# Kernel optimization log

Measured on AMD Instinct MI355X. Metric: run time of the kernel, lower is better.

Reference implementation:

```python
import jax, jax.numpy as jnp
import numpy as np

B, IN_DIM, MEM = 8192, 4096, 256
MIN_TS, MAX_TS, EPS = 0.1, 10.0, 1e-6
LN_EPS = 1e-5


def setup_inputs() -> dict:
    key = jax.random.key(0)
    ks = jax.random.split(key, 10)
    std = 0.02
    d_in = MEM + IN_DIM  # 4352
    return {
        "x": jax.random.normal(ks[0], (B, IN_DIM), jnp.float32),
        "h": jax.random.normal(ks[1], (B, MEM), jnp.float32),
        # memory_target: Linear(d_in, 2*MEM) -> LN -> GELU -> Linear(2*MEM, MEM)
        "W1": std * jax.random.normal(ks[2], (d_in, 2 * MEM), jnp.float32),
        "b1": jnp.zeros((2 * MEM,), jnp.float32),
        "g1": jnp.ones((2 * MEM,), jnp.float32),
        "be1": jnp.zeros((2 * MEM,), jnp.float32),
        "W2": std * jax.random.normal(ks[3], (2 * MEM, MEM), jnp.float32),
        "b2": jnp.zeros((MEM,), jnp.float32),
        # decay_gate: Linear(d_in, MEM) -> sigmoid
        "Wd": std * jax.random.normal(ks[4], (d_in, MEM), jnp.float32),
        "bd": jnp.zeros((MEM,), jnp.float32),
        # input_gate: Linear(d_in, MEM) -> sigmoid
        "Wu": std * jax.random.normal(ks[5], (d_in, MEM), jnp.float32),
        "bu": jnp.zeros((MEM,), jnp.float32),
    }


def _layernorm(t, g, b):
    mu = jnp.mean(t, axis=-1, keepdims=True)
    var = jnp.mean(jnp.square(t - mu), axis=-1, keepdims=True)
    return (t - mu) * jax.lax.rsqrt(var + LN_EPS) * g + b


def reference(x, h, W1, b1, g1, be1, W2, b2, Wd, bd, Wu, bu):
    combined = jnp.concatenate([h, x], axis=-1)  # [B, MEM+IN_DIM]
    # memory_target branch: Linear -> LayerNorm -> GELU (exact) -> Linear -> tanh
    t = _layernorm(combined @ W1 + b1, g1, be1)
    t = jax.nn.gelu(t, approximate=False)
    h_candidate = jnp.tanh(t @ W2 + b2)  # [B, MEM]
    # gates
    decay = jax.nn.sigmoid(combined @ Wd + bd)
    update = jax.nn.sigmoid(combined @ Wu + bu)
    decay = MIN_TS + (MAX_TS - MIN_TS) * decay + EPS
    new_h = (1.0 - update) * (h / decay) + update * h_candidate
    # normalize_memory: rescale new_h to old h's L2 norm
    h_norm = jnp.maximum(jnp.linalg.norm(h, axis=-1, keepdims=True), EPS)
    nh_norm = jnp.maximum(jnp.linalg.norm(new_h, axis=-1, keepdims=True), 1e-12)
    new_h = new_h / nh_norm * h_norm
    return new_h
```

## Files before the change

### kernel.cpp

```cpp
#include <hip/hip_runtime.h>
#include <stdint.h>

typedef unsigned short u16;

#define B_ROWS 8192
#define IN_DIM 4096
#define MEM 256
#define D_IN 4352
#define N1 1024
#define K2 512
#define LN_EPS 1e-5f

typedef __attribute__((ext_vector_type(4))) float f32x4;
typedef __attribute__((ext_vector_type(4))) uint32_t u32x4;
typedef __attribute__((ext_vector_type(4))) unsigned short u16x4;
typedef __attribute__((ext_vector_type(8))) short bf16x8;

#define AS1(p) ((__attribute__((address_space(1))) void*)(p))
#define AS3(p) ((__attribute__((address_space(3))) void*)(p))

__device__ __forceinline__ float bf2f(u16 u) {
  union { uint32_t u; float f; } c; c.u = ((uint32_t)u) << 16; return c.f;
}
__device__ __forceinline__ u16 f2bf(float f) {
  union { float f; uint32_t u; } c; c.f = f;
  uint32_t r = (c.u + 0x7fffu + ((c.u >> 16) & 1u)) >> 16;
  return (u16)r;
}
__device__ __forceinline__ uint32_t fbits(float f) {
  union { float f; uint32_t u; } c; c.f = f; return c.u;
}
__device__ __forceinline__ uint32_t pack_rne(float a, float b) {
  return ((uint32_t)f2bf(b) << 16) | f2bf(a);
}
__device__ __forceinline__ uint32_t pack_trunc(float a, float b) {
  return (fbits(b) & 0xFFFF0000u) | (fbits(a) >> 16);
}

__global__ __launch_bounds__(256)
void prep_kernel(const float* __restrict__ W1, const float* __restrict__ Wd,
                 const float* __restrict__ Wu, const float* __restrict__ W2,
                 const float* __restrict__ h, const float* __restrict__ x,
                 u16* __restrict__ WT, u16* __restrict__ W2F, u16* __restrict__ Abf) {
  __shared__ u16 tile[64][68];
  const int blk = blockIdx.x, t = threadIdx.x;
  if (blk < 1088) {
    int n0 = (blk & 15) * 64, k0 = (blk >> 4) * 64;
    const float* src; int srcN, ns0;
    if (n0 < 512)      { src = W1; srcN = 512; ns0 = n0; }
    else if (n0 < 768) { src = Wd; srcN = 256; ns0 = n0 - 512; }
    else               { src = Wu; srcN = 256; ns0 = n0 - 768; }
    int rr = t >> 4;
    int c4 = (t & 15) * 4;
#pragma unroll
    for (int i = 0; i < 4; i++) {
      int k = i * 16 + rr;
      f32x4 v = *(const f32x4*)&src[(size_t)(k0 + k) * srcN + ns0 + c4];
      tile[c4 + 0][k] = f2bf(v[0]);
      tile[c4 + 1][k] = f2bf(v[1]);
      tile[c4 + 2][k] = f2bf(v[2]);
      tile[c4 + 3][k] = f2bf(v[3]);
    }
    __syncthreads();
#pragma unroll
    for (int i = 0; i < 4; i++) {
      int n = i * 16 + rr;
      u16x4 w;
      w.x = tile[n][c4 + 0];
      w.y = tile[n][c4 + 1];
      w.z = tile[n][c4 + 2];
      w.w = tile[n][c4 + 3];
      *(u16x4*)&WT[(size_t)(n0 + n) * D_IN + k0 + c4] = w;
    }
  } else if (blk < 1104) {
    int kw = blk - 1088;
#pragma unroll
    for (int q = 0; q < 4; q++) {
      float v[8];
#pragma unroll
      for (int j = 0; j < 8; j++)
        v[j] = W2[(size_t)(kw * 32 + q * 8 + j) * 256 + t];
      u32x4 w;
      w.x = pack_rne(v[0], v[1]);
      w.y = pack_rne(v[2], v[3]);
      w.z = pack_rne(v[4], v[5]);
      w.w = pack_rne(v[6], v[7]);
      *(u32x4*)&W2F[(size_t)((kw * 4 + q) * 256 + t) * 8] = w;
    }
  } else {
    int b = blk - 1104;
    const float* src; int r, dcol;
    if (b < 1024) {
      int g = (b * 256 + t) * 8;
      src = h + g; r = g >> 8; dcol = g & 255;
    } else {
      int g = ((b - 1024) * 256 + t) * 8;
      src = x + g; r = g >> 12; dcol = MEM + (g & 4095);
    }
    f32x4 v0 = *(const f32x4*)src;
    f32x4 v1 = *(const f32x4*)(src + 4);
    u32x4 w;
    w.x = pack_rne(v0[0], v0[1]);
    w.y = pack_rne(v0[2], v0[3]);
    w.z = pack_rne(v1[0], v1[1]);
    w.w = pack_rne(v1[2], v1[3]);
    *(u32x4*)&Abf[(size_t)r * D_IN + dcol] = w;
  }
}

#define BAR() { asm volatile("" ::: "memory"); __builtin_amdgcn_s_barrier(); asm volatile("" ::: "memory"); }
#define VMW4() asm volatile("s_waitcnt vmcnt(4)" ::: "memory");
#define VMW0() asm volatile("s_waitcnt vmcnt(0)" ::: "memory");

__global__ __launch_bounds__(512, 2)
void gemm1_pre256_kernel(const u16* __restrict__ Abf, const u16* __restrict__ WT,
                         u16* __restrict__ G0, u16* __restrict__ G1, int klen) {
  __shared__ __attribute__((aligned(16))) u16 As[2][16384];
  __shared__ __attribute__((aligned(16))) u16 Bs[2][16384];
  const int t = threadIdx.x;
  const int lane = t & 63, wave = t >> 6;
  const int bid = (int)blockIdx.x;
  const int xcd = bid & 7;
  const int idx = bid >> 3;
  const int part = xcd >> 2;
  const int by = (xcd & 3) * 8 + (idx & 7);
  const int bx = idx >> 3;
  const int kbase = part * klen;
  u16* __restrict__ Gout = part ? G1 : G0;
  const int row0 = by * 256, col0 = bx * 256;
  const int q = lane >> 4, mrow = lane & 15;
  const int wm = wave >> 2, wn = wave & 3;
  const int NT = klen >> 6;

  int sr0, sc0_, sr1, sc1_;
  {
    int idx0 = t;        sr0 = idx0 >> 2; sc0_ = (idx0 & 3) ^ ((sr0 >> 1) & 3);
    int idx1 = 512 + t;  sr1 = idx1 >> 2; sc1_ = (idx1 & 3) ^ ((sr1 >> 1) & 3);
  }
  const u16* pa0 = Abf + (size_t)(row0 + sr0) * D_IN + sc0_ * 8;
  const u16* pa1 = Abf + (size_t)(row0 + sr1) * D_IN + sc1_ * 8;
  const u16* pb0 = WT  + (size_t)(col0 + sr0) * D_IN + sc0_ * 8;
  const u16* pb1 = WT  + (size_t)(col0 + sr1) * D_IN + sc1_ * 8;
  const int fsw = (mrow >> 1) & 3;

#define STAGE_A(buf, kk, kt)                                                            \
  __builtin_amdgcn_global_load_lds(AS1(pa0 + (kt) + (kk) * 32),                         \
      AS3(&As[buf][(kk) * 8192 + t * 8]), 16, 0, 0);                                    \
  __builtin_amdgcn_global_load_lds(AS1(pa1 + (kt) + (kk) * 32),                         \
      AS3(&As[buf][(kk) * 8192 + (512 + t) * 8]), 16, 0, 0);
#define STAGE_B(buf, kk, kt)                                                            \
  __builtin_amdgcn_global_load_lds(AS1(pb0 + (kt) + (kk) * 32),                         \
      AS3(&Bs[buf][(kk) * 8192 + t * 8]), 16, 0, 0);                                    \
  __builtin_amdgcn_global_load_lds(AS1(pb1 + (kt) + (kk) * 32),                         \
      AS3(&Bs[buf][(kk) * 8192 + (512 + t) * 8]), 16, 0, 0);

  f32x4 acc[8][4] = {};

  STAGE_A(0, 0, kbase)
  STAGE_B(0, 0, kbase)
  STAGE_A(0, 1, kbase)
  STAGE_B(0, 1, kbase)
  VMW4();
  BAR();

  for (int tt = 0; tt < NT; ++tt) {
    const int cur = tt & 1, nxt = cur ^ 1;
    const int kn = kbase + (tt + 1) * 64;
    const bool pf = (tt + 1 < NT);
    bf16x8 a[4], b[4];

#define READ_B(kk)                                                                      \
  _Pragma("unroll") for (int nt = 0; nt < 4; nt++) {                                    \
    int crow = wn * 64 + nt * 16 + mrow;                                                \
    b[nt] = *(const bf16x8*)&Bs[cur][(kk) * 8192 + crow * 32 + (q ^ fsw) * 8];          \
  }
#define READ_A(kk, mh)                                                                  \
  _Pragma("unroll") for (int i = 0; i < 4; i++) {                                       \
    int arow = wm * 128 + ((mh) * 4 + i) * 16 + mrow;                                   \
    a[i] = *(const bf16x8*)&As[cur][(kk) * 8192 + arow * 32 + (q ^ fsw) * 8];           \
  }
#define MFMA16(mh)                                                                      \
  __builtin_amdgcn_s_setprio(1);                                                        \
  _Pragma("unroll") for (int i = 0; i < 4; i++)                                         \
    _Pragma("unroll") for (int nt = 0; nt < 4; nt++)                                    \
      acc[(mh) * 4 + i][nt] =                                                           \
          __builtin_amdgcn_mfma_f32_16x16x32_bf16(a[i], b[nt], acc[(mh) * 4 + i][nt], 0, 0, 0); \
  __builtin_amdgcn_s_setprio(0);

    READ_B(0)
    READ_A(0, 0)
    if (pf) { STAGE_A(nxt, 0, kn) }
    BAR();
    MFMA16(0)
    BAR();
    READ_A(0, 1)
    if (pf) { STAGE_B(nxt, 0, kn) }
    BAR();
    MFMA16(1)
    if (pf) { VMW4(); } else { VMW0(); }
    BAR();
    READ_B(1)
    READ_A(1, 0)
    if (pf) { STAGE_A(nxt, 1, kn) }
    BAR();
    MFMA16(0)
    BAR();
    READ_A(1, 1)
    if (pf) { STAGE_B(nxt, 1, kn) }
    BAR();
    MFMA16(1)
    if (pf) { VMW4(); }
    BAR();
#undef READ_B
#undef READ_A
#undef MFMA16
  }

#pragma unroll
  for (int mt = 0; mt < 8; mt++) {
#pragma unroll
    for (int nt = 0; nt < 4; nt++) {
#pragma unroll
      for (int i = 0; i < 4; i++) {
        int row = row0 + wm * 128 + mt * 16 + q * 4 + i;
        int col = col0 + wn * 64 + nt * 16 + mrow;
        Gout[(size_t)row * N1 + col] = f2bf(acc[mt][nt][i]);
      }
    }
  }
}
#undef STAGE_A
#undef STAGE_B

__global__ __launch_bounds__(256, 4)
void gemm1_inline_kernel(const float* __restrict__ x, const float* __restrict__ h,
                         const u16* __restrict__ WT, u16* __restrict__ G0,
                         u16* __restrict__ G1, int klen) {
  __shared__ __attribute__((aligned(16))) u16 As[128 * 64];
  __shared__ __attribute__((aligned(16))) u16 Bs[128 * 64];
  const int t = threadIdx.x;
  const int lane = t & 63, wave = t >> 6;
  const int by = blockIdx.x & 63;
  const int bx = (blockIdx.x >> 6) & 7;
  const int part = blockIdx.x >> 9;
  const int kbase = part * klen;
  u16* __restrict__ Gout = part ? G1 : G0;
  const int row0 = by * 128, col0 = bx * 128;
  const int q = lane >> 4, mrow = lane & 15;
  const int wm = wave >> 1, wn = wave & 1;

  int ar[4], ac[4];
#pragma unroll
  for (int j = 0; j < 4; j++) {
    int idx = j * 256 + t;
    int r = idx >> 3;
    ar[j] = r;
    ac[j] = (idx & 7) ^ (r & 7);
  }
  f32x4 acc[4][4] = {};
  for (int k0 = kbase; k0 < kbase + klen; k0 += 64) {
#pragma unroll
    for (int j = 0; j < 4; j++) {
      const u16* gp = WT + (size_t)(col0 + ar[j]) * D_IN + k0 + ac[j] * 8;
      __builtin_amdgcn_global_load_lds(AS1(gp), AS3(&Bs[(j * 256 + t) * 8]), 16, 0, 0);
    }
#pragma unroll
    for (int j = 0; j < 4; j++) {
      int k = k0 + ac[j] * 8;
      const float* gp = (k < MEM) ? (h + (size_t)(row0 + ar[j]) * MEM + k)
                                  : (x + (size_t)(row0 + ar[j]) * IN_DIM + (k - MEM));
      f32x4 v0 = *(const f32x4*)gp;
      f32x4 v1 = *(const f32x4*)(gp + 4);
      u32x4 w;
      w.x = pack_trunc(v0[0], v0[1]);
      w.y = pack_trunc(v0[2], v0[3]);
      w.z = pack_trunc(v1[0], v1[1]);
      w.w = pack_trunc(v1[2], v1[3]);
      *(u32x4*)&As[(j * 256 + t) * 8] = w;
    }
    __syncthreads();
#pragma unroll
    for (int kk = 0; kk < 2; kk++) {
      bf16x8 a[4], b[4];
#pragma unroll
      for (int mt = 0; mt < 4; mt++) {
        int row = wm * 64 + mt * 16 + mrow;
        int p = (kk * 4 + q) ^ (mrow & 7);
        a[mt] = *(const bf16x8*)&As[row * 64 + p * 8];
      }
#pragma unroll
      for (int nt = 0; nt < 4; nt++) {
        int row = wn * 64 + nt * 16 + mrow;
        int p = (kk * 4 + q) ^ (mrow & 7);
        b[nt] = *(const bf16x8*)&Bs[row * 64 + p * 8];
      }
#pragma unroll
      for (int mt = 0; mt < 4; mt++) {
#pragma unroll
        for (int nt = 0; nt < 4; nt++) {
          acc[mt][nt] = __builtin_amdgcn_mfma_f32_16x16x32_bf16(a[mt], b[nt], acc[mt][nt], 0, 0, 0);
        }
      }
    }
    __syncthreads();
  }
#pragma unroll
  for (int mt = 0; mt < 4; mt++) {
#pragma unroll
    for (int nt = 0; nt < 4; nt++) {
#pragma unroll
      for (int i = 0; i < 4; i++) {
        int row = row0 + wm * 64 + mt * 16 + q * 4 + i;
        int col = col0 + wn * 64 + nt * 16 + mrow;
        Gout[(size_t)row * N1 + col] = f2bf(acc[mt][nt][i]);
      }
    }
  }
}

__global__ __launch_bounds__(256, 4)
void fused_ln_gemm2_kernel(const u16* __restrict__ G0, const u16* __restrict__ G1,
                           const u16* __restrict__ W2F, const float* __restrict__ h,
                           const float* __restrict__ b1v, const float* __restrict__ g1v,
                           const float* __restrict__ be1v, const float* __restrict__ b2,
                           const float* __restrict__ bd, const float* __restrict__ bu,
                           float* __restrict__ out, int nparts) {
  __shared__ __attribute__((aligned(16))) u16 As[16 * 512];
  __shared__ float redA[16][4], redB[16][4], scl[16];
  const int t = threadIdx.x, lane = t & 63, wave = t >> 6;
  const int q = lane >> 4, mrow = lane & 15;
  const int r0 = blockIdx.x * 16;

  {
    const int lr = t & 15;
    const int lc = t >> 4;
    float z[32];
    const u16* g0p = G0 + (size_t)(r0 + lr) * N1 + lc * 32;
    const u16* g1p = G1 + (size_t)(r0 + lr) * N1 + lc * 32;
    float s = 0.f, ss = 0.f;
#pragma unroll
    for (int j = 0; j < 4; j++) {
      u32x4 w0 = *(const u32x4*)(g0p + j * 8);
      u32x4 w1;
      if (nparts == 2) w1 = *(const u32x4*)(g1p + j * 8);
#pragma unroll
      for (int e = 0; e < 4; e++) {
        float lo = bf2f((u16)(w0[e] & 0xffff));
        float hi = bf2f((u16)(w0[e] >> 16));
        if (nparts == 2) {
          lo += bf2f((u16)(w1[e] & 0xffff));
          hi += bf2f((u16)(w1[e] >> 16));
        }
        int cb = lc * 32 + j * 8 + e * 2;
        lo += b1v[cb];
        hi += b1v[cb + 1];
        z[j * 8 + e * 2] = lo;
        z[j * 8 + e * 2 + 1] = hi;
        s += lo + hi;
        ss += lo * lo + hi * hi;
      }
    }
    s += __shfl_xor(s, 16, 64);  s += __shfl_xor(s, 32, 64);
    ss += __shfl_xor(ss, 16, 64); ss += __shfl_xor(ss, 32, 64);
    if (lane < 16) { redA[lr][wave] = s; redB[lr][wave] = ss; }
    __syncthreads();
    float S  = redA[lr][0] + redA[lr][1] + redA[lr][2] + redA[lr][3];
    float SS = redB[lr][0] + redB[lr][1] + redB[lr][2] + redB[lr][3];
    float mu = S * (1.0f / 512.0f);
    float var = SS * (1.0f / 512.0f) - mu * mu;
    float rstd = rsqrtf(var + LN_EPS);
#pragma unroll
    for (int j = 0; j < 4; j++) {
      u32x4 wpk;
#pragma unroll
      for (int e = 0; e < 4; e++) {
        int cb = lc * 32 + j * 8 + e * 2;
        float y0 = (z[j * 8 + e * 2] - mu) * rstd * g1v[cb] + be1v[cb];
        float y1 = (z[j * 8 + e * 2 + 1] - mu) * rstd * g1v[cb + 1] + be1v[cb + 1];
        float o0 = 0.5f * y0 * (1.0f + erff(y0 * 0.7071067811865475f));
        float o1 = 0.5f * y1 * (1.0f + erff(y1 * 0.7071067811865475f));
        wpk[e] = pack_rne(o0, o1);
      }
      int p = lc * 4 + j;
      int ps = p ^ (lr & 7);
      *(u32x4*)&As[lr * 512 + ps * 8] = wpk;
    }
  }
  __syncthreads();

  f32x4 acc[4] = {};
#pragma unroll
  for (int kw = 0; kw < 16; kw++) {
    int pa = (kw * 4 + q) ^ (mrow & 7);
    bf16x8 a = *(const bf16x8*)&As[mrow * 512 + pa * 8];
#pragma unroll
    for (int nt = 0; nt < 4; nt++) {
      const u16* bp = W2F + (size_t)((kw * 4 + q) * 256 + wave * 64 + nt * 16 + mrow) * 8;
      bf16x8 b = *(const bf16x8*)bp;
      acc[nt] = __builtin_amdgcn_mfma_f32_16x16x32_bf16(a, b, acc[nt], 0, 0, 0);
    }
  }
  __syncthreads();

  float snh[4], shh[4];
#pragma unroll
  for (int i = 0; i < 4; i++) {
    int r = q * 4 + i;
    size_t grow = (size_t)(r0 + r);
    float a_nh = 0.f, a_h = 0.f;
#pragma unroll
    for (int nt = 0; nt < 4; nt++) {
      int c = wave * 64 + nt * 16 + mrow;
      float hc = tanhf(acc[nt][i] + b2[c]);
      float zd = bf2f(G0[grow * N1 + 512 + c]);
      float zu = bf2f(G0[grow * N1 + 768 + c]);
      if (nparts == 2) {
        zd += bf2f(G1[grow * N1 + 512 + c]);
        zu += bf2f(G1[grow * N1 + 768 + c]);
      }
      zd += bd[c];
      zu += bu[c];
      float dec = 0.1f + 9.9f / (1.0f + expf(-zd)) + 1e-6f;
      float u = 1.0f / (1.0f + expf(-zu));
      float hv = h[grow * MEM + c];
      float nh = (1.0f - u) * (hv / dec) + u * hc;
      acc[nt][i] = nh;
      a_nh += nh * nh;
      a_h += hv * hv;
    }
    snh[i] = a_nh;
    shh[i] = a_h;
  }
#pragma unroll
  for (int m = 1; m <= 8; m <<= 1) {
#pragma unroll
    for (int i = 0; i < 4; i++) {
      snh[i] += __shfl_xor(snh[i], m, 64);
      shh[i] += __shfl_xor(shh[i], m, 64);
    }
  }
  if (mrow == 0) {
#pragma unroll
    for (int i = 0; i < 4; i++) {
      int r = q * 4 + i;
      redA[r][wave] = snh[i];
      redB[r][wave] = shh[i];
    }
  }
  __syncthreads();
  if (t < 16) {
    float tn = redA[t][0] + redA[t][1] + redA[t][2] + redA[t][3];
    float th = redB[t][0] + redB[t][1] + redB[t][2] + redB[t][3];
    float hn = fmaxf(sqrtf(th), 1e-6f);
    float nn = fmaxf(sqrtf(tn), 1e-12f);
    scl[t] = hn / nn;
  }
  __syncthreads();
#pragma unroll
  for (int i = 0; i < 4; i++) {
    int r = q * 4 + i;
    size_t grow = (size_t)(r0 + r);
    float sc = scl[r];
#pragma unroll
    for (int nt = 0; nt < 4; nt++) {
      int c = wave * 64 + nt * 16 + mrow;
      out[grow * MEM + c] = acc[nt][i] * sc;
    }
  }
}

extern "C" void kernel_launch(void* const* d_in, const int* in_sizes, int n_in,
                              void* d_out, int out_size, void* d_ws, size_t ws_size,
                              hipStream_t stream) {
  const float* x   = (const float*)d_in[0];
  const float* h   = (const float*)d_in[1];
  const float* W1  = (const float*)d_in[2];
  const float* b1  = (const float*)d_in[3];
  const float* g1  = (const float*)d_in[4];
  const float* be1 = (const float*)d_in[5];
  const float* W2  = (const float*)d_in[6];
  const float* b2  = (const float*)d_in[7];
  const float* Wd  = (const float*)d_in[8];
  const float* bd  = (const float*)d_in[9];
  const float* Wu  = (const float*)d_in[10];
  const float* bu  = (const float*)d_in[11];
  float* out = (float*)d_out;

  char* ws = (char*)d_ws;
  u16* WT  = (u16*)(ws);
  u16* W2F = (u16*)(ws + 8912896);
  u16* G0  = (u16*)(ws + 9175040);
  u16* G1  = (u16*)(ws + 25952256);
  u16* Abf = (u16*)(ws + 42729472);

  const int nparts = (ws_size >= 42729472u) ? 2 : 1;
  const int klen = D_IN / nparts;
  const bool use_pre = (ws_size >= 114032640u) && (nparts == 2);

  if (use_pre) {
    prep_kernel<<<18512, 256, 0, stream>>>(W1, Wd, Wu, W2, h, x, WT, W2F, Abf);
    gemm1_pre256_kernel<<<256, 512, 0, stream>>>(Abf, WT, G0, G1, klen);
  } else {
    prep_kernel<<<1104, 256, 0, stream>>>(W1, Wd, Wu, W2, h, x, WT, W2F, Abf);
    gemm1_inline_kernel<<<512 * nparts, 256, 0, stream>>>(x, h, WT, G0, G1, klen);
  }

  fused_ln_gemm2_kernel<<<B_ROWS / 16, 256, 0, stream>>>(G0, G1, W2F, h, b1, g1, be1,
                                                         b2, bd, bu, out, nparts);
}
```

Baseline: 339.1 us.

## Pre-swizzle weights into MFMA fragment layout and load B directly to registers

The prep kernel now writes the transposed weight matrix in a fragment-major layout, so each wave's MFMA B operand is one contiguous 16-byte-per-lane global load. The pre256 GEMM drops the B shared-memory tile and its staging, double-buffers B fragments in registers, and cuts the per-iteration barriers to one. This removes LDS traffic and barrier overhead for B but makes B reads depend on global or L2 latency, with each wave re-fetching its own fragments, and it raises register pressure.

```diff
diff --git a/kernel.cpp b/kernel.cpp
--- a/kernel.cpp
+++ b/kernel.cpp
@@ -41,7 +41,8 @@
 void prep_kernel(const float* __restrict__ W1, const float* __restrict__ Wd,
                  const float* __restrict__ Wu, const float* __restrict__ W2,
                  const float* __restrict__ h, const float* __restrict__ x,
-                 u16* __restrict__ WT, u16* __restrict__ W2F, u16* __restrict__ Abf) {
+                 u16* __restrict__ WT, u16* __restrict__ W2F, u16* __restrict__ Abf,
+                 int pre) {
   __shared__ u16 tile[64][68];
   const int blk = blockIdx.x, t = threadIdx.x;
   if (blk < 1088) {
@@ -70,7 +71,16 @@
       w.y = tile[n][c4 + 1];
       w.z = tile[n][c4 + 2];
       w.w = tile[n][c4 + 3];
-      *(u16x4*)&WT[(size_t)(n0 + n) * D_IN + k0 + c4] = w;
+      if (pre) {
+        int n16 = (n0 >> 4) + i;
+        int kg = k0 + c4;
+        int kstep = kg >> 5;
+        int qq = (kg >> 3) & 3;
+        int j0 = kg & 7;
+        *(u16x4*)&WT[((size_t)(kstep * 64 + n16) * 64 + qq * 16 + rr) * 8 + j0] = w;
+      } else {
+        *(u16x4*)&WT[(size_t)(n0 + n) * D_IN + k0 + c4] = w;
+      }
     }
   } else if (blk < 1104) {
     int kw = blk - 1088;
@@ -110,13 +120,11 @@
 
 #define BAR() { asm volatile("" ::: "memory"); __builtin_amdgcn_s_barrier(); asm volatile("" ::: "memory"); }
 #define VMW4() asm volatile("s_waitcnt vmcnt(4)" ::: "memory");
-#define VMW0() asm volatile("s_waitcnt vmcnt(0)" ::: "memory");
 
 __global__ __launch_bounds__(512, 2)
-void gemm1_pre256_kernel(const u16* __restrict__ Abf, const u16* __restrict__ WT,
+void gemm1_pre256_kernel(const u16* __restrict__ Abf, const u16* __restrict__ WTF,
                          u16* __restrict__ G0, u16* __restrict__ G1, int klen) {
   __shared__ __attribute__((aligned(16))) u16 As[2][16384];
-  __shared__ __attribute__((aligned(16))) u16 Bs[2][16384];
   const int t = threadIdx.x;
   const int lane = t & 63, wave = t >> 6;
   const int bid = (int)blockIdx.x;
@@ -139,8 +147,6 @@
   }
   const u16* pa0 = Abf + (size_t)(row0 + sr0) * D_IN + sc0_ * 8;
   const u16* pa1 = Abf + (size_t)(row0 + sr1) * D_IN + sc1_ * 8;
-  const u16* pb0 = WT  + (size_t)(col0 + sr0) * D_IN + sc0_ * 8;
-  const u16* pb1 = WT  + (size_t)(col0 + sr1) * D_IN + sc1_ * 8;
   const int fsw = (mrow >> 1) & 3;
 
 #define STAGE_A(buf, kk, kt)                                                            \
@@ -148,18 +154,16 @@
       AS3(&As[buf][(kk) * 8192 + t * 8]), 16, 0, 0);                                    \
   __builtin_amdgcn_global_load_lds(AS1(pa1 + (kt) + (kk) * 32),                         \
       AS3(&As[buf][(kk) * 8192 + (512 + t) * 8]), 16, 0, 0);
-#define STAGE_B(buf, kk, kt)                                                            \
-  __builtin_amdgcn_global_load_lds(AS1(pb0 + (kt) + (kk) * 32),                         \
-      AS3(&Bs[buf][(kk) * 8192 + t * 8]), 16, 0, 0);                                    \
-  __builtin_amdgcn_global_load_lds(AS1(pb1 + (kt) + (kk) * 32),                         \
-      AS3(&Bs[buf][(kk) * 8192 + (512 + t) * 8]), 16, 0, 0);
+
+  const u16* bptr = WTF + (size_t)(kbase >> 5) * 32768 + (bx * 16 + wn * 4) * 512 + lane * 8;
 
   f32x4 acc[8][4] = {};
+  bf16x8 b0[4], b1[4];
 
   STAGE_A(0, 0, kbase)
-  STAGE_B(0, 0, kbase)
   STAGE_A(0, 1, kbase)
-  STAGE_B(0, 1, kbase)
+#pragma unroll
+  for (int nt = 0; nt < 4; nt++) b0[nt] = *(const bf16x8*)(bptr + nt * 512);
   VMW4();
   BAR();
 
@@ -167,51 +171,48 @@
     const int cur = tt & 1, nxt = cur ^ 1;
     const int kn = kbase + (tt + 1) * 64;
     const bool pf = (tt + 1 < NT);
-    bf16x8 a[4], b[4];
-
-#define READ_B(kk)                                                                      \
-  _Pragma("unroll") for (int nt = 0; nt < 4; nt++) {                                    \
-    int crow = wn * 64 + nt * 16 + mrow;                                                \
-    b[nt] = *(const bf16x8*)&Bs[cur][(kk) * 8192 + crow * 32 + (q ^ fsw) * 8];          \
-  }
-#define READ_A(kk, mh)                                                                  \
+
+#pragma unroll
+    for (int nt = 0; nt < 4; nt++) b1[nt] = *(const bf16x8*)(bptr + 32768 + nt * 512);
+    if (pf) { STAGE_A(nxt, 0, kn) }
+
+#define READ_A(kk, mh, areg)                                                            \
   _Pragma("unroll") for (int i = 0; i < 4; i++) {                                       \
     int arow = wm * 128 + ((mh) * 4 + i) * 16 + mrow;                                   \
-    a[i] = *(const bf16x8*)&As[cur][(kk) * 8192 + arow * 32 + (q ^ fsw) * 8];           \
-  }
-#define MFMA16(mh)                                                                      \
+    areg[i] = *(const bf16x8*)&As[cur][(kk) * 8192 + arow * 32 + (q ^ fsw) * 8];        \
+  }
+#define MFMA16(mh, breg)                                                                \
   __builtin_amdgcn_s_setprio(1);                                                        \
   _Pragma("unroll") for (int i = 0; i < 4; i++)                                         \
     _Pragma("unroll") for (int nt = 0; nt < 4; nt++)                                    \
       acc[(mh) * 4 + i][nt] =                                                           \
-          __builtin_amdgcn_mfma_f32_16x16x32_bf16(a[i], b[nt], acc[(mh) * 4 + i][nt], 0, 0, 0); \
+          __builtin_amdgcn_mfma_f32_16x16x32_bf16(a[i], breg[nt], acc[(mh) * 4 + i][nt], 0, 0, 0); \
   __builtin_amdgcn_s_setprio(0);
 
-    READ_B(0)
-    READ_A(0, 0)
-    if (pf) { STAGE_A(nxt, 0, kn) }
-    BAR();
-    MFMA16(0)
-    BAR();
-    READ_A(0, 1)
-    if (pf) { STAGE_B(nxt, 0, kn) }
-    BAR();
-    MFMA16(1)
-    if (pf) { VMW4(); } else { VMW0(); }
-    BAR();
-    READ_B(1)
-    READ_A(1, 0)
-    if (pf) { STAGE_A(nxt, 1, kn) }
-    BAR();
-    MFMA16(0)
-    BAR();
-    READ_A(1, 1)
-    if (pf) { STAGE_B(nxt, 1, kn) }
-    BAR();
-    MFMA16(1)
-    if (pf) { VMW4(); }
-    BAR();
-#undef READ_B
+    {
+      bf16x8 a[4];
+      READ_A(0, 0, a)
+      MFMA16(0, b0)
+      READ_A(0, 1, a)
+      MFMA16(1, b0)
+    }
+    if (pf) {
+      STAGE_A(nxt, 1, kn)
+#pragma unroll
+      for (int nt = 0; nt < 4; nt++) b0[nt] = *(const bf16x8*)(bptr + 65536 + nt * 512);
+    }
+    {
+      bf16x8 a[4];
+      READ_A(1, 0, a)
+      MFMA16(0, b1)
+      READ_A(1, 1, a)
+      MFMA16(1, b1)
+    }
+    if (pf) {
+      VMW4();
+      BAR();
+    }
+    bptr += 65536;
 #undef READ_A
 #undef MFMA16
   }
@@ -230,7 +231,6 @@
   }
 }
 #undef STAGE_A
-#undef STAGE_B
 
 __global__ __launch_bounds__(256, 4)
 void gemm1_inline_kernel(const float* __restrict__ x, const float* __restrict__ h,
@@ -498,10 +498,10 @@
   const bool use_pre = (ws_size >= 114032640u) && (nparts == 2);
 
   if (use_pre) {
-    prep_kernel<<<18512, 256, 0, stream>>>(W1, Wd, Wu, W2, h, x, WT, W2F, Abf);
+    prep_kernel<<<18512, 256, 0, stream>>>(W1, Wd, Wu, W2, h, x, WT, W2F, Abf, 1);
     gemm1_pre256_kernel<<<256, 512, 0, stream>>>(Abf, WT, G0, G1, klen);
   } else {
-    prep_kernel<<<1104, 256, 0, stream>>>(W1, Wd, Wu, W2, h, x, WT, W2F, Abf);
+    prep_kernel<<<1104, 256, 0, stream>>>(W1, Wd, Wu, W2, h, x, WT, W2F, Abf, 0);
     gemm1_inline_kernel<<<512 * nparts, 256, 0, stream>>>(x, h, WT, G0, G1, klen);
   }
 
```

New measurement: 346.5 us. 1.02x slower.

## Simplify GEMM1 double-buffer pipeline to one prefetch and one barrier per tile

Applied to the files above, without the earlier changes.

Replaces the fine-grained interleaved schedule, which staged async global-to-LDS loads between MFMA groups with many barriers and explicit vmcnt waits, with a simpler loop. Each iteration now issues all next-tile loads up front, runs all LDS reads and MFMAs, then ends with one __syncthreads. The aim is to cut barrier overhead and let the compiler schedule freely. The risk is losing precise control of load/compute overlap, and that __syncthreads may wait on all outstanding loads at every tile.

```diff
diff --git a/kernel.cpp b/kernel.cpp
--- a/kernel.cpp
+++ b/kernel.cpp
@@ -107,10 +107,6 @@
     *(u32x4*)&Abf[(size_t)r * D_IN + dcol] = w;
   }
 }
-
-#define BAR() { asm volatile("" ::: "memory"); __builtin_amdgcn_s_barrier(); asm volatile("" ::: "memory"); }
-#define VMW4() asm volatile("s_waitcnt vmcnt(4)" ::: "memory");
-#define VMW0() asm volatile("s_waitcnt vmcnt(0)" ::: "memory");
 
 __global__ __launch_bounds__(512, 2)
 void gemm1_pre256_kernel(const u16* __restrict__ Abf, const u16* __restrict__ WT,
@@ -157,17 +153,21 @@
   f32x4 acc[8][4] = {};
 
   STAGE_A(0, 0, kbase)
+  STAGE_A(0, 1, kbase)
   STAGE_B(0, 0, kbase)
-  STAGE_A(0, 1, kbase)
   STAGE_B(0, 1, kbase)
-  VMW4();
-  BAR();
+  __syncthreads();
 
   for (int tt = 0; tt < NT; ++tt) {
     const int cur = tt & 1, nxt = cur ^ 1;
     const int kn = kbase + (tt + 1) * 64;
-    const bool pf = (tt + 1 < NT);
-    bf16x8 a[4], b[4];
+
+    if (tt + 1 < NT) {
+      STAGE_A(nxt, 0, kn)
+      STAGE_A(nxt, 1, kn)
+      STAGE_B(nxt, 0, kn)
+      STAGE_B(nxt, 1, kn)
+    }
 
 #define READ_B(kk)                                                                      \
   _Pragma("unroll") for (int nt = 0; nt < 4; nt++) {                                    \
@@ -187,33 +187,24 @@
           __builtin_amdgcn_mfma_f32_16x16x32_bf16(a[i], b[nt], acc[(mh) * 4 + i][nt], 0, 0, 0); \
   __builtin_amdgcn_s_setprio(0);
 
-    READ_B(0)
-    READ_A(0, 0)
-    if (pf) { STAGE_A(nxt, 0, kn) }
-    BAR();
-    MFMA16(0)
-    BAR();
-    READ_A(0, 1)
-    if (pf) { STAGE_B(nxt, 0, kn) }
-    BAR();
-    MFMA16(1)
-    if (pf) { VMW4(); } else { VMW0(); }
-    BAR();
-    READ_B(1)
-    READ_A(1, 0)
-    if (pf) { STAGE_A(nxt, 1, kn) }
-    BAR();
-    MFMA16(0)
-    BAR();
-    READ_A(1, 1)
-    if (pf) { STAGE_B(nxt, 1, kn) }
-    BAR();
-    MFMA16(1)
-    if (pf) { VMW4(); }
-    BAR();
+    {
+      bf16x8 a[4], b[4];
+      READ_B(0)
+      READ_A(0, 0)
+      MFMA16(0)
+      READ_A(0, 1)
+      MFMA16(1)
+      READ_B(1)
+      READ_A(1, 0)
+      MFMA16(0)
+      READ_A(1, 1)
+      MFMA16(1)
+    }
 #undef READ_B
 #undef READ_A
 #undef MFMA16
+
+    __syncthreads();
   }
 
 #pragma unroll
```

Result: slower. 350.9 us (+3.5%).
